# Optimization experiments

Hardware: AMD Instinct MI355X
Metric: run time of the kernel (lower is better)

## Reference

```python
import jax, jax.numpy as jnp
import numpy as np

B, N, E = 2, 2048, 1024   # batch, seq_len, embed_dim (= hidden_dim)
H, HD = 16, 64            # num_heads, head_dim


def setup_inputs() -> dict:
    key = jax.random.key(0)
    ks = jax.random.split(key, 6)
    w = lambda k: jax.random.normal(k, (E, E), jnp.float32) * 0.02
    return {
        "x": jax.random.normal(ks[0], (B, N, E), jnp.float32),
        "Wq": w(ks[1]), "bq": jnp.zeros((E,), jnp.float32),
        "Wk": w(ks[2]), "bk": jnp.zeros((E,), jnp.float32),
        "Wv": w(ks[3]), "bv": jnp.zeros((E,), jnp.float32),
        "Wu": w(ks[4]), "bu": jnp.zeros((E,), jnp.float32),
        "Wo": w(ks[5]), "bo": jnp.zeros((E,), jnp.float32),
        "ln_g": jnp.ones((E,), jnp.float32),
        "ln_b": jnp.zeros((E,), jnp.float32),
    }


def reference(x, Wq, bq, Wk, bk, Wv, bv, Wu, bu, Wo, bo, ln_g, ln_b):
    # projections (torch Linear: x @ W.T + b)
    q = x @ Wq.T + bq
    k = x @ Wk.T + bk
    v = jax.nn.silu(x @ Wv.T + bv)   # uv_act = swish
    u = jax.nn.silu(x @ Wu.T + bu)
    # split heads: [B, N, H*HD] -> [B, H, N, HD]
    split = lambda t: t.reshape(B, N, H, HD).transpose(0, 2, 1, 3)
    q, k, v = split(q), split(k), split(v)
    # non-softmax attention: ReLU on scaled energy (no causal mask)
    energy = jnp.einsum("bhnd,bhmd->bhnm", q, k) / jnp.float32(np.sqrt(HD))
    energy = jax.nn.relu(energy)
    out = jnp.einsum("bhnm,bhmd->bhnd", energy, v)
    # merge heads: [B, H, N, HD] -> [B, N, H*HD]
    out = out.transpose(0, 2, 1, 3).reshape(B, N, H * HD)
    # layernorm over hidden_dim
    mu = out.mean(-1, keepdims=True)
    var = out.var(-1, keepdims=True)
    out = (out - mu) * jax.lax.rsqrt(var + 1e-5) * ln_g + ln_b
    # gate and output projection
    out = u * out
    return out @ Wo.T + bo
```

## Files before the change

kernel.cpp:

```cpp
#include <hip/hip_runtime.h>
#include <stdint.h>

typedef unsigned short u16;
typedef __attribute__((ext_vector_type(8))) short short8;
typedef __attribute__((ext_vector_type(4))) short short4v;
typedef __attribute__((ext_vector_type(4))) float floatx4;
typedef __attribute__((ext_vector_type(4))) int intx4;

#define B_ 2
#define N_ 2048
#define E_ 1024
#define H_ 16
#define HD_ 64
#define M_TOT (B_ * N_)

__device__ __forceinline__ float bf2f(u16 h) {
    union { unsigned u; float f; } c; c.u = ((unsigned)h) << 16; return c.f;
}
__device__ __forceinline__ u16 f2bf(float f) {
    union { float f; unsigned u; } c; c.f = f;
    unsigned r = c.u + 0x7FFFu + ((c.u >> 16) & 1u);
    return (u16)(r >> 16);
}
__device__ __forceinline__ float silu_f(float x) { return x / (1.f + __expf(-x)); }

template <typename T> __device__ __forceinline__ void store_out(T* p, float v);
template <> __device__ __forceinline__ void store_out<u16>(u16* p, float v)    { *p = f2bf(v); }
template <> __device__ __forceinline__ void store_out<float>(float* p, float v) { *p = v; }

__device__ __forceinline__ void gll16(const void* g, void* l) {
    __builtin_amdgcn_global_load_lds(
        (const __attribute__((address_space(1))) void*)g,
        (__attribute__((address_space(3))) void*)l,
        16, 0, 0);
}

__device__ __forceinline__ short4v relu_pack(floatx4 s) {
    union { float f; unsigned u; } c0, c1, c2, c3;
    c0.f = fmaxf(s[0], 0.f); c1.f = fmaxf(s[1], 0.f);
    c2.f = fmaxf(s[2], 0.f); c3.f = fmaxf(s[3], 0.f);
    unsigned lo = __builtin_amdgcn_perm(c1.u + 0x8000u, c0.u + 0x8000u, 0x07060302);
    unsigned hi = __builtin_amdgcn_perm(c3.u + 0x8000u, c2.u + 0x8000u, 0x07060302);
    union { unsigned v[2]; short4v s4; } r; r.v[0] = lo; r.v[1] = hi;
    return r.s4;
}

__launch_bounds__(256, 4)
__global__ void cvt6(const float* __restrict__ s0, const float* __restrict__ s1,
                     const float* __restrict__ s2, const float* __restrict__ s3,
                     const float* __restrict__ s4, const float* __restrict__ s5,
                     u16* __restrict__ d0, u16* __restrict__ d1,
                     u16* __restrict__ d2, u16* __restrict__ d3,
                     u16* __restrict__ d4, u16* __restrict__ d5)
{
    const int z = blockIdx.z;
    if (z > 0 && blockIdx.x >= E_ * E_ / 2048) return;
    const float* src = (z == 0) ? s0 : (z == 1) ? s1 : (z == 2) ? s2
                     : (z == 3) ? s3 : (z == 4) ? s4 : s5;
    u16* dst         = (z == 0) ? d0 : (z == 1) ? d1 : (z == 2) ? d2
                     : (z == 3) ? d3 : (z == 4) ? d4 : d5;
    const int i = (blockIdx.x * 256 + threadIdx.x) * 8;
    floatx4 a = *(const floatx4*)(src + i);
    floatx4 b = *(const floatx4*)(src + i + 4);
    union { u16 h[8]; intx4 v; } o;
    o.h[0] = f2bf(a[0]); o.h[1] = f2bf(a[1]); o.h[2] = f2bf(a[2]); o.h[3] = f2bf(a[3]);
    o.h[4] = f2bf(b[0]); o.h[5] = f2bf(b[1]); o.h[6] = f2bf(b[2]); o.h[7] = f2bf(b[3]);
    *(intx4*)(dst + i) = o.v;
}

__launch_bounds__(256, 3)
__global__ void gemm_pipe(const u16* __restrict__ A,
                          const u16* __restrict__ W0, const u16* __restrict__ W1,
                          const u16* __restrict__ W2, const u16* __restrict__ W3,
                          const float* __restrict__ bi0, const float* __restrict__ bi1,
                          const float* __restrict__ bi2, const float* __restrict__ bi3,
                          u16* __restrict__ O0, u16* __restrict__ O1,
                          u16* __restrict__ O2, u16* __restrict__ O3,
                          int actmask, int scalemask, int K)
{
    __shared__ u16 a_lds[3][128 * 32];
    __shared__ u16 b_lds[3][128 * 32];

    const int z = blockIdx.z;
    const u16* W    = (z == 0) ? W0 : (z == 1) ? W1 : (z == 2) ? W2 : W3;
    const float* Bi = (z == 0) ? bi0 : (z == 1) ? bi1 : (z == 2) ? bi2 : bi3;
    u16* Out        = (z == 0) ? O0 : (z == 1) ? O1 : (z == 2) ? O2 : O3;
    const bool act = (actmask >> z) & 1;
    const float osc = ((scalemask >> z) & 1) ? 0.125f : 1.0f;

    const int t    = threadIdx.x;
    const int wave = t >> 6, lane = t & 63, quad = lane >> 4, l16 = lane & 15;
    const int wm = wave >> 1, wn = wave & 1;
    const int m0 = blockIdx.y * 128;
    const int n0 = blockIdx.x * 128;

    floatx4 acc[4][4];
    const floatx4 fz = {0.f, 0.f, 0.f, 0.f};
#pragma unroll
    for (int i = 0; i < 4; i++)
#pragma unroll
        for (int j = 0; j < 4; j++) acc[i][j] = fz;

    const int ar = t >> 2;
    const int ac = (t & 3) * 8;
    const u16* Ag0 = A + (size_t)(m0 + ar) * K + ac;
    const u16* Ag1 = A + (size_t)(m0 + 64 + ar) * K + ac;
    const u16* Bg0 = W + (size_t)(n0 + ar) * K + ac;
    const u16* Bg1 = W + (size_t)(n0 + 64 + ar) * K + ac;

    const int nt = K / 32;

#define PSTAGE(tt, bi) {                                           \
        gll16(Ag0 + (tt) * 32, &a_lds[bi][wave * 512]);            \
        gll16(Ag1 + (tt) * 32, &a_lds[bi][2048 + wave * 512]);     \
        gll16(Bg0 + (tt) * 32, &b_lds[bi][wave * 512]);            \
        gll16(Bg1 + (tt) * 32, &b_lds[bi][2048 + wave * 512]); }

    PSTAGE(0, 0);
    PSTAGE(1, 1);
    asm volatile("s_waitcnt vmcnt(4)" ::: "memory");
    __builtin_amdgcn_s_barrier();

    for (int tt = 0; tt < nt; tt++) {
        const int bi = tt % 3;
        if (tt + 2 < nt) {
            PSTAGE(tt + 2, (tt + 2) % 3);
        }
        short8 af[4], bfr[4];
#pragma unroll
        for (int i = 0; i < 4; i++)
            af[i]  = *(const short8*)&a_lds[bi][(wm * 64 + i * 16 + l16) * 32 + quad * 8];
#pragma unroll
        for (int j = 0; j < 4; j++)
            bfr[j] = *(const short8*)&b_lds[bi][(wn * 64 + j * 16 + l16) * 32 + quad * 8];
#pragma unroll
        for (int i = 0; i < 4; i++)
#pragma unroll
            for (int j = 0; j < 4; j++)
                acc[i][j] = __builtin_amdgcn_mfma_f32_16x16x32_bf16(af[i], bfr[j], acc[i][j], 0, 0, 0);
        if (tt + 2 < nt) {
            asm volatile("s_waitcnt vmcnt(4)" ::: "memory");
        } else {
            asm volatile("s_waitcnt vmcnt(0)" ::: "memory");
        }
        __builtin_amdgcn_s_barrier();
    }
#undef PSTAGE

    float bias_v[4];
#pragma unroll
    for (int j = 0; j < 4; j++) bias_v[j] = Bi[n0 + wn * 64 + j * 16 + l16];

#pragma unroll
    for (int i = 0; i < 4; i++) {
        const int row = m0 + wm * 64 + i * 16 + quad * 4;
#pragma unroll
        for (int j = 0; j < 4; j++) {
            const int col = n0 + wn * 64 + j * 16 + l16;
#pragma unroll
            for (int r = 0; r < 4; r++) {
                float v = acc[i][j][r] + bias_v[j];
                if (act) v = silu_f(v);
                v *= osc;
                Out[(size_t)(row + r) * E_ + col] = f2bf(v);
            }
        }
    }
}

__launch_bounds__(256, 2)
__global__ void gemm_out(const u16* __restrict__ A, const u16* __restrict__ W,
                         const float* __restrict__ Bi, float* __restrict__ Out,
                         int K)
{
    __shared__ u16 a_lds[3][64 * 32];
    __shared__ u16 b_lds[3][128 * 32];

    const int t    = threadIdx.x;
    const int wave = t >> 6, lane = t & 63, quad = lane >> 4, l16 = lane & 15;
    const int m0 = blockIdx.y * 64;
    const int n0 = blockIdx.x * 128;

    floatx4 acc[4][2];
    const floatx4 fz = {0.f, 0.f, 0.f, 0.f};
    for (int i = 0; i < 4; i++)
        for (int j = 0; j < 2; j++) acc[i][j] = fz;

    const int ar = t >> 2;
    const int ac = (t & 3) * 8;
    const u16* Ag0 = A + (size_t)(m0 + ar) * K + ac;
    const u16* Bg0 = W + (size_t)(n0 + ar) * K + ac;
    const u16* Bg1 = W + (size_t)(n0 + 64 + ar) * K + ac;

    const int nt = K / 32;

#define GO_STAGE(tt, bi) {                                      \
        gll16(Ag0 + (tt) * 32, &a_lds[bi][wave * 512]);         \
        gll16(Bg0 + (tt) * 32, &b_lds[bi][wave * 512]);         \
        gll16(Bg1 + (tt) * 32, &b_lds[bi][2048 + wave * 512]); }

    GO_STAGE(0, 0);
    GO_STAGE(1, 1);
    asm volatile("s_waitcnt vmcnt(3)" ::: "memory");
    __builtin_amdgcn_s_barrier();

    for (int tt = 0; tt < nt; tt++) {
        const int bi = tt % 3;
        if (tt + 2 < nt) {
            GO_STAGE(tt + 2, (tt + 2) % 3);
        }
        short8 af[4], bfr[2];
#pragma unroll
        for (int i = 0; i < 4; i++)
            af[i]  = *(const short8*)&a_lds[bi][(i * 16 + l16) * 32 + quad * 8];
#pragma unroll
        for (int j = 0; j < 2; j++)
            bfr[j] = *(const short8*)&b_lds[bi][(wave * 32 + j * 16 + l16) * 32 + quad * 8];
#pragma unroll
        for (int i = 0; i < 4; i++)
#pragma unroll
            for (int j = 0; j < 2; j++)
                acc[i][j] = __builtin_amdgcn_mfma_f32_16x16x32_bf16(af[i], bfr[j], acc[i][j], 0, 0, 0);
        if (tt + 2 < nt) {
            asm volatile("s_waitcnt vmcnt(3)" ::: "memory");
        } else {
            asm volatile("s_waitcnt vmcnt(0)" ::: "memory");
        }
        __builtin_amdgcn_s_barrier();
    }
#undef GO_STAGE

    float bias_v[2];
    for (int j = 0; j < 2; j++) bias_v[j] = Bi[n0 + wave * 32 + j * 16 + l16];

    for (int i = 0; i < 4; i++) {
        const int row = m0 + i * 16 + quad * 4;
        for (int j = 0; j < 2; j++) {
            const int col = n0 + wave * 32 + j * 16 + l16;
            for (int r = 0; r < 4; r++)
                Out[(size_t)(row + r) * E_ + col] = acc[i][j][r] + bias_v[j];
        }
    }
}

#define LK 72
#define LV 72
#define KSPLIT 2
#define KCHUNK (N_ / KSPLIT)
#define NKT (KCHUNK / 64)

__launch_bounds__(256, 2)
__global__ void attn(const u16* __restrict__ Q, const u16* __restrict__ Kk,
                     const u16* __restrict__ V,
                     u16* __restrict__ P0, u16* __restrict__ P1)
{
    __shared__ u16 k_lds[2][64 * LK];
    __shared__ u16 v_lds[2][64 * LV];

    const int bh = blockIdx.y;
    const int b = bh >> 4, h = bh & 15;
    const int z = blockIdx.z;
    u16* __restrict__ Oa = (z == 0) ? P0 : P1;
    const int key_base = z * KCHUNK;

    const int t = threadIdx.x;
    const int wave = t >> 6, lane = t & 63, quad = lane >> 4, l16 = lane & 15;
    const int q0 = blockIdx.x * 256 + wave * 64;
    const size_t base = (size_t)b * N_ * E_ + h * HD_;

    short8 aq[4][2];
    for (int mi = 0; mi < 4; mi++)
        for (int ks = 0; ks < 2; ks++)
            aq[mi][ks] = *(const short8*)(Q + base + (size_t)(q0 + mi * 16 + l16) * E_ + ks * 32 + quad * 8);

    floatx4 o[4][4];
    const floatx4 fz = {0.f, 0.f, 0.f, 0.f};
    for (int mi = 0; mi < 4; mi++)
        for (int nd = 0; nd < 4; nd++) o[mi][nd] = fz;

    const int srow = t >> 2, sseg = (t & 3) * 16;
    const int prow = (srow & 32) + (((srow >> 2) & 1) << 4)
                   + (((srow >> 3) & 3) << 2) + (srow & 3);
    const u16* Ksrc = Kk + base + (size_t)(key_base + srow) * E_ + sseg;
    const u16* Vsrc = V + base + (size_t)(key_base + srow) * E_ + sseg;
    const int kofs = prow * LK + sseg;

    intx4 kv0 = *(const intx4*)(Ksrc);
    intx4 kv1 = *(const intx4*)(Ksrc + 8);
    intx4 vv0 = *(const intx4*)(Vsrc);
    intx4 vv1 = *(const intx4*)(Vsrc + 8);
    {
        *(intx4*)(&k_lds[0][kofs])     = kv0;
        *(intx4*)(&k_lds[0][kofs + 8]) = kv1;
        const u16* v0p = (const u16*)&vv0;
        const u16* v1p = (const u16*)&vv1;
        for (int i = 0; i < 8; i++) {
            v_lds[0][(sseg + i) * LV + srow]     = v0p[i];
            v_lds[0][(sseg + 8 + i) * LV + srow] = v1p[i];
        }
    }

    for (int kt = 0; kt < NKT; kt++) {
        __syncthreads();
        const int cur = kt & 1;

        if (kt + 1 < NKT) {
            const u16* kg = Ksrc + (size_t)((kt + 1) * 64) * E_;
            const u16* vg = Vsrc + (size_t)((kt + 1) * 64) * E_;
            kv0 = *(const intx4*)(kg);
            kv1 = *(const intx4*)(kg + 8);
            vv0 = *(const intx4*)(vg);
            vv1 = *(const intx4*)(vg + 8);
        }

        for (int g = 0; g < 2; g++) {
            short8 ka[2][2];
            for (int tp = 0; tp < 2; tp++)
                for (int ks = 0; ks < 2; ks++)
                    ka[tp][ks] = *(const short8*)&k_lds[cur][(g * 32 + tp * 16 + l16) * LK + ks * 32 + quad * 8];
            short8 bv[4];
            for (int nd = 0; nd < 4; nd++)
                bv[nd] = *(const short8*)&v_lds[cur][(nd * 16 + l16) * LV + g * 32 + quad * 8];

            for (int mi = 0; mi < 4; mi++) {
                floatx4 c0 = __builtin_amdgcn_mfma_f32_16x16x32_bf16(ka[0][0], aq[mi][0], fz, 0, 0, 0);
                c0 = __builtin_amdgcn_mfma_f32_16x16x32_bf16(ka[0][1], aq[mi][1], c0, 0, 0, 0);
                floatx4 c1 = __builtin_amdgcn_mfma_f32_16x16x32_bf16(ka[1][0], aq[mi][0], fz, 0, 0, 0);
                c1 = __builtin_amdgcn_mfma_f32_16x16x32_bf16(ka[1][1], aq[mi][1], c1, 0, 0, 0);
                union { short4v h[2]; short8 s8; } sf;
                sf.h[0] = relu_pack(c0);
                sf.h[1] = relu_pack(c1);
                for (int nd = 0; nd < 4; nd++)
                    o[mi][nd] = __builtin_amdgcn_mfma_f32_16x16x32_bf16(sf.s8, bv[nd], o[mi][nd], 0, 0, 0);
            }
        }

        if (kt + 1 < NKT) {
            const int nxt = cur ^ 1;
            *(intx4*)(&k_lds[nxt][kofs])     = kv0;
            *(intx4*)(&k_lds[nxt][kofs + 8]) = kv1;
            const u16* v0p = (const u16*)&vv0;
            const u16* v1p = (const u16*)&vv1;
            for (int i = 0; i < 8; i++) {
                v_lds[nxt][(sseg + i) * LV + srow]     = v0p[i];
                v_lds[nxt][(sseg + 8 + i) * LV + srow] = v1p[i];
            }
        }
    }

    for (int mi = 0; mi < 4; mi++)
        for (int nd = 0; nd < 4; nd++)
            for (int r = 0; r < 4; r++)
                Oa[(size_t)(b * N_ + q0 + mi * 16 + quad * 4 + r) * E_ + h * HD_ + nd * 16 + l16] =
                    f2bf(o[mi][nd][r]);
}

__launch_bounds__(256, 4)
__global__ void ln_gate(const u16* __restrict__ P0, const u16* __restrict__ P1,
                        const u16* __restrict__ U,
                        const float* __restrict__ G, const float* __restrict__ Bb,
                        u16* __restrict__ Out)
{
    const int row = blockIdx.x;
    const int t = threadIdx.x;
    const size_t idx = (size_t)row * E_ + t * 4;
    const short4v a0 = *(const short4v*)(P0 + idx);
    const short4v a1 = *(const short4v*)(P1 + idx);
    floatx4 v;
    for (int i = 0; i < 4; i++)
        v[i] = bf2f((u16)a0[i]) + bf2f((u16)a1[i]);
    float s  = v[0] + v[1] + v[2] + v[3];
    float ss = v[0] * v[0] + v[1] * v[1] + v[2] * v[2] + v[3] * v[3];
    for (int off = 32; off; off >>= 1) {
        s  += __shfl_down(s, off, 64);
        ss += __shfl_down(ss, off, 64);
    }
    __shared__ float red[8];
    const int wave = t >> 6, lane = t & 63;
    if (lane == 0) { red[wave] = s; red[4 + wave] = ss; }
    __syncthreads();
    const float S  = red[0] + red[1] + red[2] + red[3];
    const float SS = red[4] + red[5] + red[6] + red[7];
    const float mu  = S * (1.f / E_);
    const float var = SS * (1.f / E_) - mu * mu;
    const float rstd = rsqrtf(var + 1e-5f);

    short4v outv;
    for (int i = 0; i < 4; i++) {
        const int e = t * 4 + i;
        float y = (v[i] - mu) * rstd * G[e] + Bb[e];
        y *= bf2f(U[idx + i]);
        outv[i] = (short)f2bf(y);
    }
    *(short4v*)(Out + idx) = outv;
}

extern "C" void kernel_launch(void* const* d_in, const int* in_sizes, int n_in,
                              void* d_out, int out_size, void* d_ws, size_t ws_size,
                              hipStream_t stream)
{
    const float* x   = (const float*)d_in[0];
    const float* Wq  = (const float*)d_in[1];
    const float* bq  = (const float*)d_in[2];
    const float* Wk  = (const float*)d_in[3];
    const float* bk  = (const float*)d_in[4];
    const float* Wv  = (const float*)d_in[5];
    const float* bv  = (const float*)d_in[6];
    const float* Wu  = (const float*)d_in[7];
    const float* bu  = (const float*)d_in[8];
    const float* Wo  = (const float*)d_in[9];
    const float* bo  = (const float*)d_in[10];
    const float* lng = (const float*)d_in[11];
    const float* lnb = (const float*)d_in[12];

    char* ws = (char*)d_ws;
    u16*  qw  = (u16*)(ws);
    u16*  kw  = (u16*)(ws + 8388608);
    u16*  vw  = (u16*)(ws + 16777216);
    u16*  uw  = (u16*)(ws + 25165824);
    u16*  p0  = (u16*)(ws + 33554432);
    u16*  p1  = (u16*)(ws + 41943040);
    u16*  xb  = (u16*)(ws + 50331648);
    u16*  wbq = (u16*)(ws + 58720256);
    u16*  wbk = (u16*)(ws + 60817408);
    u16*  wbv = (u16*)(ws + 62914560);
    u16*  wbu = (u16*)(ws + 65011712);
    u16*  wbo = (u16*)(ws + 67108864);
    u16*  gw  = (u16*)(ws);

    float* out = (float*)d_out;

    cvt6<<<dim3(M_TOT * E_ / 2048, 1, 6), dim3(256, 1, 1), 0, stream>>>(
        x, Wq, Wk, Wv, Wu, Wo, xb, wbq, wbk, wbv, wbu, wbo);
    gemm_pipe<<<dim3(8, 32, 4), dim3(256, 1, 1), 0, stream>>>(
        xb, wbq, wbk, wbv, wbu, bq, bk, bv, bu, qw, kw, vw, uw, 0xC, 0x1, E_);
    attn<<<dim3(N_ / 256, B_ * H_, KSPLIT), dim3(256, 1, 1), 0, stream>>>(qw, kw, vw, p0, p1);
    ln_gate<<<dim3(M_TOT, 1, 1), dim3(256, 1, 1), 0, stream>>>(p0, p1, uw, lng, lnb, gw);
    gemm_out<<<dim3(E_ / 128, M_TOT / 64, 1), dim3(256, 1, 1), 0, stream>>>(gw, wbo, bo, out, E_);
}
```

Before: 226.5 us.

## Replace pipelined projection GEMM with single-buffer templated GEMM and XCD block swizzle

```diff
diff --git a/kernel.cpp b/kernel.cpp
--- a/kernel.cpp
+++ b/kernel.cpp
@@ -68,37 +68,41 @@
     *(intx4*)(dst + i) = o.v;
 }
 
-__launch_bounds__(256, 3)
-__global__ void gemm_pipe(const u16* __restrict__ A,
-                          const u16* __restrict__ W0, const u16* __restrict__ W1,
-                          const u16* __restrict__ W2, const u16* __restrict__ W3,
-                          const float* __restrict__ bi0, const float* __restrict__ bi1,
-                          const float* __restrict__ bi2, const float* __restrict__ bi3,
-                          u16* __restrict__ O0, u16* __restrict__ O1,
-                          u16* __restrict__ O2, u16* __restrict__ O3,
-                          int actmask, int scalemask, int K)
-{
-    __shared__ u16 a_lds[3][128 * 32];
-    __shared__ u16 b_lds[3][128 * 32];
-
-    const int z = blockIdx.z;
+template <typename OutT>
+__launch_bounds__(256, 2)
+__global__ void gemm4(const u16* __restrict__ A,
+                      const u16* __restrict__ W0, const u16* __restrict__ W1,
+                      const u16* __restrict__ W2, const u16* __restrict__ W3,
+                      const float* __restrict__ bi0, const float* __restrict__ bi1,
+                      const float* __restrict__ bi2, const float* __restrict__ bi3,
+                      OutT* __restrict__ O0, OutT* __restrict__ O1,
+                      OutT* __restrict__ O2, OutT* __restrict__ O3,
+                      int actmask, int scalemask, int K)
+{
+    __shared__ u16 a_lds[128 * 32];
+    __shared__ u16 b_lds[128 * 32];
+
+    const int lin = blockIdx.x + blockIdx.y * 8 + blockIdx.z * 256;
+    const int swz = (lin & 7) * 128 + (lin >> 3);
+    const int z   = swz >> 8;
+    const int by  = (swz >> 3) & 31;
+    const int bx  = swz & 7;
+
     const u16* W    = (z == 0) ? W0 : (z == 1) ? W1 : (z == 2) ? W2 : W3;
     const float* Bi = (z == 0) ? bi0 : (z == 1) ? bi1 : (z == 2) ? bi2 : bi3;
-    u16* Out        = (z == 0) ? O0 : (z == 1) ? O1 : (z == 2) ? O2 : O3;
+    OutT* Out       = (z == 0) ? O0 : (z == 1) ? O1 : (z == 2) ? O2 : O3;
     const bool act = (actmask >> z) & 1;
     const float osc = ((scalemask >> z) & 1) ? 0.125f : 1.0f;
 
     const int t    = threadIdx.x;
     const int wave = t >> 6, lane = t & 63, quad = lane >> 4, l16 = lane & 15;
     const int wm = wave >> 1, wn = wave & 1;
-    const int m0 = blockIdx.y * 128;
-    const int n0 = blockIdx.x * 128;
+    const int m0 = by * 128;
+    const int n0 = bx * 128;
 
     floatx4 acc[4][4];
     const floatx4 fz = {0.f, 0.f, 0.f, 0.f};
-#pragma unroll
     for (int i = 0; i < 4; i++)
-#pragma unroll
         for (int j = 0; j < 4; j++) acc[i][j] = fz;
 
     const int ar = t >> 2;
@@ -107,62 +111,41 @@
     const u16* Ag1 = A + (size_t)(m0 + 64 + ar) * K + ac;
     const u16* Bg0 = W + (size_t)(n0 + ar) * K + ac;
     const u16* Bg1 = W + (size_t)(n0 + 64 + ar) * K + ac;
-
-    const int nt = K / 32;
-
-#define PSTAGE(tt, bi) {                                           \
-        gll16(Ag0 + (tt) * 32, &a_lds[bi][wave * 512]);            \
-        gll16(Ag1 + (tt) * 32, &a_lds[bi][2048 + wave * 512]);     \
-        gll16(Bg0 + (tt) * 32, &b_lds[bi][wave * 512]);            \
-        gll16(Bg1 + (tt) * 32, &b_lds[bi][2048 + wave * 512]); }
-
-    PSTAGE(0, 0);
-    PSTAGE(1, 1);
-    asm volatile("s_waitcnt vmcnt(4)" ::: "memory");
-    __builtin_amdgcn_s_barrier();
-
-    for (int tt = 0; tt < nt; tt++) {
-        const int bi = tt % 3;
-        if (tt + 2 < nt) {
-            PSTAGE(tt + 2, (tt + 2) % 3);
-        }
+    u16* al0 = a_lds + wave * 512;
+    u16* al1 = a_lds + 2048 + wave * 512;
+    u16* bl0 = b_lds + wave * 512;
+    u16* bl1 = b_lds + 2048 + wave * 512;
+
+    for (int k0 = 0; k0 < K; k0 += 32) {
+        __syncthreads();
+        gll16(Ag0 + k0, al0);
+        gll16(Ag1 + k0, al1);
+        gll16(Bg0 + k0, bl0);
+        gll16(Bg1 + k0, bl1);
+        __syncthreads();
+
         short8 af[4], bfr[4];
-#pragma unroll
         for (int i = 0; i < 4; i++)
-            af[i]  = *(const short8*)&a_lds[bi][(wm * 64 + i * 16 + l16) * 32 + quad * 8];
-#pragma unroll
+            af[i]  = *(const short8*)&a_lds[(wm * 64 + i * 16 + l16) * 32 + quad * 8];
         for (int j = 0; j < 4; j++)
-            bfr[j] = *(const short8*)&b_lds[bi][(wn * 64 + j * 16 + l16) * 32 + quad * 8];
-#pragma unroll
+            bfr[j] = *(const short8*)&b_lds[(wn * 64 + j * 16 + l16) * 32 + quad * 8];
         for (int i = 0; i < 4; i++)
-#pragma unroll
             for (int j = 0; j < 4; j++)
                 acc[i][j] = __builtin_amdgcn_mfma_f32_16x16x32_bf16(af[i], bfr[j], acc[i][j], 0, 0, 0);
-        if (tt + 2 < nt) {
-            asm volatile("s_waitcnt vmcnt(4)" ::: "memory");
-        } else {
-            asm volatile("s_waitcnt vmcnt(0)" ::: "memory");
-        }
-        __builtin_amdgcn_s_barrier();
-    }
-#undef PSTAGE
+    }
 
     float bias_v[4];
-#pragma unroll
     for (int j = 0; j < 4; j++) bias_v[j] = Bi[n0 + wn * 64 + j * 16 + l16];
 
-#pragma unroll
     for (int i = 0; i < 4; i++) {
         const int row = m0 + wm * 64 + i * 16 + quad * 4;
-#pragma unroll
         for (int j = 0; j < 4; j++) {
             const int col = n0 + wn * 64 + j * 16 + l16;
-#pragma unroll
             for (int r = 0; r < 4; r++) {
                 float v = acc[i][j][r] + bias_v[j];
                 if (act) v = silu_f(v);
                 v *= osc;
-                Out[(size_t)(row + r) * E_ + col] = f2bf(v);
+                store_out<OutT>(&Out[(size_t)(row + r) * E_ + col], v);
             }
         }
     }
@@ -257,15 +240,19 @@
     __shared__ u16 k_lds[2][64 * LK];
     __shared__ u16 v_lds[2][64 * LV];
 
-    const int bh = blockIdx.y;
+    const int lin = blockIdx.x + blockIdx.y * 8 + blockIdx.z * 256;
+    const int swz = (lin & 7) * 64 + (lin >> 3);
+    const int z   = swz >> 8;
+    const int bh  = (swz >> 3) & 31;
+    const int qb  = swz & 7;
+
     const int b = bh >> 4, h = bh & 15;
-    const int z = blockIdx.z;
     u16* __restrict__ Oa = (z == 0) ? P0 : P1;
     const int key_base = z * KCHUNK;
 
     const int t = threadIdx.x;
     const int wave = t >> 6, lane = t & 63, quad = lane >> 4, l16 = lane & 15;
-    const int q0 = blockIdx.x * 256 + wave * 64;
+    const int q0 = qb * 256 + wave * 64;
     const size_t base = (size_t)b * N_ * E_ + h * HD_;
 
     short8 aq[4][2];
@@ -432,7 +419,7 @@
 
     cvt6<<<dim3(M_TOT * E_ / 2048, 1, 6), dim3(256, 1, 1), 0, stream>>>(
         x, Wq, Wk, Wv, Wu, Wo, xb, wbq, wbk, wbv, wbu, wbo);
-    gemm_pipe<<<dim3(8, 32, 4), dim3(256, 1, 1), 0, stream>>>(
+    gemm4<u16><<<dim3(8, 32, 4), dim3(256, 1, 1), 0, stream>>>(
         xb, wbq, wbk, wbv, wbu, bq, bk, bv, bu, qw, kw, vw, uw, 0xC, 0x1, E_);
     attn<<<dim3(N_ / 256, B_ * H_, KSPLIT), dim3(256, 1, 1), 0, stream>>>(qw, kw, vw, p0, p1);
     ln_gate<<<dim3(M_TOT, 1, 1), dim3(256, 1, 1), 0, stream>>>(p0, p1, uw, lng, lnb, gw);
```

Measured after the change: 213.4 us. 1.06x faster.
